# Kernel tuning notes

Hardware: AMD Instinct MI355X
Metric: run time of the kernel (lower is better)

Reference implementation:

```python
import jax, jax.numpy as jnp
import numpy as np

SEQ, BATCH = 256, 8
N_NODES = SEQ * BATCH
VOCAB, D_MODEL, H, D_K, D_FF, N_LAYERS, MAX_POS = 259, 256, 8, 32, 1024, 2, 128


def setup_inputs() -> dict:
    key = jax.random.key(0)
    ks = jax.random.split(key, 16)
    # structured causal edge list per sequence (dst attends to src <= dst, incl. self)
    tri_dst, tri_src = np.tril_indices(SEQ)
    offs = (np.arange(BATCH) * SEQ)[:, None]
    edge_src = jnp.asarray((tri_src[None, :] + offs).ravel(), dtype=jnp.int64)
    edge_dst = jnp.asarray((tri_dst[None, :] + offs).ravel(), dtype=jnp.int64)
    positions = jnp.tile(jnp.arange(SEQ, dtype=jnp.int64), BATCH)
    tokens = jax.random.randint(ks[0], (N_NODES,), 0, VOCAB, dtype=jnp.int64)
    s = 0.02
    p = lambda k, shp: jax.random.normal(k, shp, dtype=jnp.float32) * s
    return {
        "tokens": tokens, "positions": positions,
        "edge_src": edge_src, "edge_dst": edge_dst,
        "coord_emb": p(ks[1], (3, D_MODEL)),
        "pos_emb": p(ks[2], (MAX_POS, D_MODEL)),
        "value_emb": p(ks[3], (VOCAB, D_MODEL)),
        "ln1_scale": jnp.ones((N_LAYERS, D_MODEL)), "ln1_bias": jnp.zeros((N_LAYERS, D_MODEL)),
        "Wqkv": p(ks[4], (N_LAYERS, D_MODEL, 3 * D_MODEL)),
        "Wo": p(ks[5], (N_LAYERS, D_MODEL, D_MODEL)),
        "ln2_scale": jnp.ones((N_LAYERS, D_MODEL)), "ln2_bias": jnp.zeros((N_LAYERS, D_MODEL)),
        "W1": p(ks[6], (N_LAYERS, D_MODEL, D_FF)), "b1": jnp.zeros((N_LAYERS, D_FF)),
        "W2": p(ks[7], (N_LAYERS, D_FF, D_MODEL)), "b2": jnp.zeros((N_LAYERS, D_MODEL)),
        "lnf_scale": jnp.ones((D_MODEL,)), "lnf_bias": jnp.zeros((D_MODEL,)),
        "Wg": p(ks[8], (D_MODEL, VOCAB)), "bg": jnp.zeros((VOCAB,)),
    }


def _ln(x, scale, bias, eps=1e-5):
    mu = jnp.mean(x, axis=-1, keepdims=True)
    var = jnp.var(x, axis=-1, keepdims=True)
    return (x - mu) * jax.lax.rsqrt(var + eps) * scale + bias


def _graph_attention(x, src, dst, Wqkv, Wo, ln_s, ln_b):
    n = x.shape[0]
    xn = _ln(x, ln_s, ln_b)
    qkv = (xn @ Wqkv).reshape(n, 3, H, D_K)
    q, k, v = qkv[:, 0], qkv[:, 1], qkv[:, 2]  # [n, H, D_K] each
    # u_dot_v('k','q','score') per edge, scaled
    score = jnp.einsum("ehd,ehd->eh", k[src], q[dst]) / jnp.sqrt(jnp.float32(D_K))
    # edge_softmax over incoming edges of each dst node
    smax = jax.ops.segment_max(score, dst, num_segments=n)      # [n, H]
    ex = jnp.exp(score - smax[dst])                              # [E, H]
    denom = jax.ops.segment_sum(ex, dst, num_segments=n)        # [n, H]
    alpha = ex / denom[dst]
    # u_mul_e('v','softmax_score') + sum reduce -> z on dst nodes
    z = jax.ops.segment_sum(alpha[:, :, None] * v[src], dst, num_segments=n)  # [n, H, D_K]
    return x + z.reshape(n, D_MODEL) @ Wo


def reference(tokens, positions, edge_src, edge_dst, coord_emb, pos_emb, value_emb,
              ln1_scale, ln1_bias, Wqkv, Wo, ln2_scale, ln2_bias, W1, b1, W2, b2,
              lnf_scale, lnf_bias, Wg, bg):
    x = coord_emb[positions % 3] + pos_emb[positions // 3] + value_emb[tokens]
    for i in range(Wqkv.shape[0]):
        x = _graph_attention(x, edge_src, edge_dst, Wqkv[i], Wo[i], ln1_scale[i], ln1_bias[i])
        h = _ln(x, ln2_scale[i], ln2_bias[i])
        x = x + jax.nn.relu(h @ W1[i] + b1[i]) @ W2[i] + b2[i]
    out = _ln(x, lnf_scale, lnf_bias) @ Wg + bg
    return jax.nn.log_softmax(out, axis=-1)
```

## Files before the change

### kernel.cpp

```cpp
#include <hip/hip_runtime.h>
#include <hip/hip_bf16.h>

typedef __hip_bfloat16 bf16;
typedef unsigned short ushort_t;
typedef unsigned int uint_t;
typedef __attribute__((ext_vector_type(8))) short short8;
typedef __attribute__((ext_vector_type(4))) float floatx4;

#define D_MODEL 256
#define SEQ     256
#define BATCH   8
#define NN      2048
#define NHEAD   8
#define DK      32
#define DFF     1024
#define VOCAB   259
#define NLAYER  2

#define WQKVT_OFF 0
#define WOT_OFF   393216
#define W1T_OFF   524288
#define W2T_OFF   1048576
#define WGT_OFF   1572864
#define WT_TOTAL  1639168
// ... 143 lines not shown

template<bool BF, bool I64>
__device__ void prep_body(const void* tok, const void* pos,
        const void* ce, const void* pe, const void* ve,
        const void* Wqkv,
        const void* ln1s, const void* ln1b, const void* ln2s, const void* ln2b,
        const void* lnfs, const void* lnfb,
        const void* b1, const void* b2, const void* bg,
        ushort_t* WT, float* lnP, float* bP, float* x, ushort_t* xn,
        ushort_t (*tile)[72]) {
    int blk = blockIdx.x;
    if (blk < 48) {
        int lo = blk;
        ttile<BF>(Wqkv, 0, 256, 768, lo/12, lo%12, WT + WQKVT_OFF, tile);
    } else if (blk < 70) {
        int gid = (blk - 48) * 256 + threadIdx.x;
        if (gid < LNP_TOTAL) {
            float v;
            if      (gid < 512)  v = ldw<BF>(ln1s, gid);
            else if (gid < 1024) v = ldw<BF>(ln1b, gid - 512);
            else if (gid < 1536) v = ldw<BF>(ln2s, gid - 1024);
            else if (gid < 2048) v = ldw<BF>(ln2b, gid - 1536);
            else if (gid < 2304) v = ldw<BF>(lnfs, gid - 2048);
            else                 v = ldw<BF>(lnfb, gid - 2304);
            lnP[gid] = v;
        } else if (gid < LNP_TOTAL + BP_TOTAL) {
            int g = gid - LNP_TOTAL;
            float v;
            if      (g < 2048) v = ldw<BF>(b1, g);
            else if (g < 2560) v = ldw<BF>(b2, g - 2048);
            else               v = ldw<BF>(bg, g - 2560);
            bP[g] = v;
        }
    } else {
        embedln16<BF, I64>(tok, pos, ce, pe, ve, ln1s, ln1b, (blk - 70) * 16, x, xn);
    }
}

__global__ void __launch_bounds__(256) prep_k(const void* tok, const void* pos,
        const void* ce, const void* pe, const void* ve,
        const void* Wqkv,
        const void* ln1s, const void* ln1b, const void* ln2s, const void* ln2b,
        const void* lnfs, const void* lnfb,
        const void* b1, const void* b2, const void* bg,
        ushort_t* WT, float* lnP, float* bP, float* x, ushort_t* xn) {
    __shared__ ushort_t tile[64][72];
    bool BF = detBF(ln1s), I64 = detI64(pos);
    if (BF) { if (I64) prep_body<true,true >(tok,pos,ce,pe,ve,Wqkv,ln1s,ln1b,ln2s,ln2b,lnfs,lnfb,b1,b2,bg,WT,lnP,bP,x,xn,tile);
              else     prep_body<true,false>(tok,pos,ce,pe,ve,Wqkv,ln1s,ln1b,ln2s,ln2b,lnfs,lnfb,b1,b2,bg,WT,lnP,bP,x,xn,tile); }
    else    { if (I64) prep_body<false,true >(tok,pos,ce,pe,ve,Wqkv,ln1s,ln1b,ln2s,ln2b,lnfs,lnfb,b1,b2,bg,WT,lnP,bP,x,xn,tile);
              else     prep_body<false,false>(tok,pos,ce,pe,ve,Wqkv,ln1s,ln1b,ln2s,ln2b,lnfs,lnfb,b1,b2,bg,WT,lnP,bP,x,xn,tile); }
}

template<bool BF>
__device__ void qkvt_body(const ushort_t* __restrict__ xn,
        const ushort_t* __restrict__ WqkvT0, ushort_t* __restrict__ qkvB,
        const void* Wqkv, const void* Wo, const void* W1, const void* W2, const void* Wg,
        ushort_t* WT, ushort_t (*tile)[72]) {
    int bid = blockIdx.x;
    if (bid < 384) {
        int t = threadIdx.x;
        int lane = t & 63, wave = t >> 6;
        int quad = lane >> 4, l16 = lane & 15;
        int wm = (wave >> 1) * 32, wn = (wave & 1) * 32;
        int rowBase = (bid & 31) * 64, colBase = (bid >> 5) * 64;
        floatx4 acc[2][2];
        #pragma unroll
        for (int a = 0; a < 2; ++a)
            #pragma unroll
            for (int b = 0; b < 2; ++b) acc[a][b] = (floatx4){0.f,0.f,0.f,0.f};
        const ushort_t* a0 = xn + (size_t)(rowBase + wm + l16) * 256 + quad * 8;
        const ushort_t* a1 = a0 + (size_t)16 * 256;
        const ushort_t* b0 = WqkvT0 + (size_t)(colBase + wn + l16) * 256 + quad * 8;
        const ushort_t* b1 = b0 + (size_t)16 * 256;
        #pragma unroll 8
        for (int k0 = 0; k0 < 256; k0 += 32) {
            short8 af0 = *reinterpret_cast<const short8*>(a0 + k0);
            short8 af1 = *reinterpret_cast<const short8*>(a1 + k0);
            short8 bf0 = *reinterpret_cast<const short8*>(b0 + k0);
            short8 bf1 = *reinterpret_cast<const short8*>(b1 + k0);
            acc[0][0] = __builtin_amdgcn_mfma_f32_16x16x32_bf16(af0, bf0, acc[0][0], 0,0,0);
            acc[0][1] = __builtin_amdgcn_mfma_f32_16x16x32_bf16(af0, bf1, acc[0][1], 0,0,0);
            acc[1][0] = __builtin_amdgcn_mfma_f32_16x16x32_bf16(af1, bf0, acc[1][0], 0,0,0);
            acc[1][1] = __builtin_amdgcn_mfma_f32_16x16x32_bf16(af1, bf1, acc[1][1], 0,0,0);
        }
        #pragma unroll
        for (int nt = 0; nt < 2; ++nt) {
            int col = colBase + wn + nt*16 + l16;
            #pragma unroll
            for (int mt = 0; mt < 2; ++mt)
                #pragma unroll
                for (int r = 0; r < 4; ++r) {
                    int row = rowBase + wm + mt*16 + quad*4 + r;
                    qkvB[(size_t)row * 768 + col] = f2bs(acc[mt][nt][r]);
                }
        }
    } else {
        int task = bid - 384;
        const void* src; int K, N, tk, tn; size_t dstOff, srcOff;
        if (task < 48)       { int lo = task; src=Wqkv; K=256; N=768;
                               srcOff=196608; dstOff=WQKVT_OFF+196608;
                               tk=lo/12; tn=lo%12; }
        else if (task < 80)  { int t2=task-48, L=t2/16, lo=t2%16; src=Wo; K=256; N=256;
                               srcOff=(size_t)L*65536; dstOff=WOT_OFF+(size_t)L*65536;
                               tk=lo/4; tn=lo%4; }
        else if (task < 208) { int t2=task-80, L=t2/64, lo=t2%64; src=W1; K=256; N=1024;
                               srcOff=(size_t)L*262144; dstOff=W1T_OFF+(size_t)L*262144;
                               tk=lo/16; tn=lo%16; }
        else if (task < 336) { int t2=task-208, L=t2/64, lo=t2%64; src=W2; K=1024; N=256;
                               srcOff=(size_t)L*262144; dstOff=W2T_OFF+(size_t)L*262144;
                               tk=lo/4; tn=lo%4; }
        else                 { int lo=task-336; src=Wg; K=256; N=259;
                               srcOff=0; dstOff=WGT_OFF; tk=lo/5; tn=lo%5; }
        ttile<BF>(src, srcOff, K, N, tk, tn, WT + dstOff, tile);
    }
}

__global__ void __launch_bounds__(256) qkvt_k(const ushort_t* __restrict__ xn,
        const ushort_t* __restrict__ WqkvT0, ushort_t* __restrict__ qkvB,
        const void* Wqkv, const void* Wo, const void* W1, const void* W2, const void* Wg,
        ushort_t* WT, const void* ln1s) {
    __shared__ ushort_t tile[64][72];
    if (detBF(ln1s)) qkvt_body<true >(xn, WqkvT0, qkvB, Wqkv, Wo, W1, W2, Wg, WT, tile);
    else             qkvt_body<false>(xn, WqkvT0, qkvB, Wqkv, Wo, W1, W2, Wg, WT, tile);
}

union AttnSH {
    struct {
        ushort_t Ks[SEQ][40];
        ushort_t Qs[64][40];
    } a;
    ushort_t Ps[64][264];
};
__global__ void __launch_bounds__(256) attn_k(const ushort_t* __restrict__ qkvB,
                                              ushort_t* __restrict__ zB,
                                              float* __restrict__ yZ) {
    __shared__ AttnSH u;
    __shared__ ushort_t Vt[32][264];
    int t = threadIdx.x;
    {
        float4 z4 = make_float4(0.f, 0.f, 0.f, 0.f);
        float4* yp = reinterpret_cast<float4*>(yZ + (size_t)blockIdx.x * 2048);
        yp[t]       = z4;
        yp[t + 256] = z4;
    }
    int lane = t & 63, wave = t >> 6;
    int quad = lane >> 4, l16 = lane & 15;
    int tile = blockIdx.x & 3, bh = blockIdx.x >> 2;
    int b = bh >> 3, h = bh & 7;
    int base = b * SEQ;
    int dstBase = tile * 64;
    int tileEnd = (tile + 1) * 64;

    int nV = tileEnd * 4;
    for (int i = t; i < nV; i += 256) {
        int src = i >> 2, g = i & 3;
        const ushort_t* rp = qkvB + (size_t)(base + src) * 768 + h * 32 + g * 8;
        uint4 kv = *reinterpret_cast<const uint4*>(rp + 256);
        *reinterpret_cast<uint4*>(&u.a.Ks[src][g * 8]) = kv;
        uint4 vv = *reinterpret_cast<const uint4*>(rp + 512);
        const ushort_t* vs = (const ushort_t*)&vv;
        #pragma unroll
        for (int j = 0; j < 8; ++j) Vt[g * 8 + j][src] = vs[j];
    }
    {
        int r = t >> 2, g = t & 3;
        uint4 qv = *reinterpret_cast<const uint4*>(
            qkvB + (size_t)(base + dstBase + r) * 768 + h * 32 + g * 8);
        *reinterpret_cast<uint4*>(&u.a.Qs[r][g * 8]) = qv;
    }
    __syncthreads();

    const float scale = 0.17677669529663687f;
    int stLim = tile * 4 + wave;
    int stCnt = stLim + 1;
    short8 qf = *reinterpret_cast<const short8*>(&u.a.Qs[wave * 16 + l16][quad * 8]);
    floatx4 accs[16];
    #pragma unroll
    for (int st = 0; st < 16; ++st) {
        if (st <= stLim) {
            short8 kf = *reinterpret_cast<const short8*>(&u.a.Ks[st * 16 + l16][quad * 8]);
            accs[st] = __builtin_amdgcn_mfma_f32_16x16x32_bf16(qf, kf, (floatx4){0.f,0.f,0.f,0.f}, 0, 0, 0);
        }
    }
    float mrow[4] = {-3e38f, -3e38f, -3e38f, -3e38f};
    #pragma unroll
    for (int st = 0; st < 16; ++st) {
        if (st <= stLim) {
            int srcg = st * 16 + l16;
            #pragma unroll
            for (int r = 0; r < 4; ++r) {
                int dstg = dstBase + wave * 16 + quad * 4 + r;
                float sv = (srcg <= dstg) ? accs[st][r] * scale : -3e38f;
                accs[st][r] = sv;
                mrow[r] = fmaxf(mrow[r], sv);
            }
        }
    }
    #pragma unroll
    for (int mk = 1; mk < 16; mk <<= 1)
        #pragma unroll
        for (int r = 0; r < 4; ++r) mrow[r] = fmaxf(mrow[r], __shfl_xor(mrow[r], mk, 64));
    float lrow[4] = {0.f, 0.f, 0.f, 0.f};
    #pragma unroll
    for (int st = 0; st < 16; ++st) {
        if (st <= stLim) {
            #pragma unroll
            for (int r = 0; r < 4; ++r) {
                float p = __expf(accs[st][r] - mrow[r]);
                accs[st][r] = p;
                lrow[r] += p;
            }
        }
    }
    #pragma unroll
    for (int mk = 1; mk < 16; mk <<= 1)
        #pragma unroll
        for (int r = 0; r < 4; ++r) lrow[r] += __shfl_xor(lrow[r], mk, 64);
    __syncthreads();

    #pragma unroll
    for (int st = 0; st < 16; ++st) {
        if (st <= stLim) {
            #pragma unroll
            for (int r = 0; r < 4; ++r)
                u.Ps[wave * 16 + quad * 4 + r][st * 16 + l16] = f2bs(accs[st][r]);
        }
    }
    if (stCnt & 1) {
        #pragma unroll
        for (int r = 0; r < 4; ++r)
            u.Ps[wave * 16 + quad * 4 + r][stCnt * 16 + l16] = 0;
    }
    __syncthreads();

    int ktCnt = (stCnt + 1) >> 1;
    floatx4 acco[2];
    acco[0] = (floatx4){0.f,0.f,0.f,0.f};
    acco[1] = (floatx4){0.f,0.f,0.f,0.f};
    #pragma unroll
    for (int kt = 0; kt < 8; ++kt) {
        if (kt < ktCnt) {
            short8 pf = *reinterpret_cast<const short8*>(&u.Ps[wave * 16 + l16][kt * 32 + quad * 8]);
            #pragma unroll
            for (int dn = 0; dn < 2; ++dn) {
                short8 vf = *reinterpret_cast<const short8*>(&Vt[dn * 16 + l16][kt * 32 + quad * 8]);
                acco[dn] = __builtin_amdgcn_mfma_f32_16x16x32_bf16(pf, vf, acco[dn], 0, 0, 0);
            }
        }
    }
    #pragma unroll
    for (int dn = 0; dn < 2; ++dn)
        #pragma unroll
        for (int r = 0; r < 4; ++r)
            zB[(size_t)(base + dstBase + wave * 16 + quad * 4 + r) * 256
               + h * 32 + dn * 16 + l16] = f2bs(acco[dn][r] / lrow[r]);
}

__global__ void __launch_bounds__(256) tail_k(
        const ushort_t* __restrict__ zB, const ushort_t* __restrict__ WoT,
        const float* __restrict__ xIn,
        const float* __restrict__ ls2, const float* __restrict__ lb2,
        const ushort_t* __restrict__ W1T, const float* __restrict__ b1P,
        const ushort_t* __restrict__ W2T, const float* __restrict__ b2P,
        float* __restrict__ yAcc) {
    __shared__ float    xrowS[32][256];
    __shared__ ushort_t xnA[32][264];
    ushort_t (*hmidS)[264] = reinterpret_cast<ushort_t (*)[264]>(&xrowS[0][0]);
    int t = threadIdx.x, lane = t & 63, wave = t >> 6;
    int quad = lane >> 4, l16 = lane & 15;
    int rowBase = blockIdx.x * 32, cg = blockIdx.y;
    float vpre[2][4][4];

    {
        floatx4 acc[2][4];
        #pragma unroll
        for (int mt = 0; mt < 2; ++mt)
            #pragma unroll
            for (int nt = 0; nt < 4; ++nt) acc[mt][nt] = (floatx4){0.f,0.f,0.f,0.f};
        const ushort_t* a0 = zB + (size_t)(rowBase + l16) * 256 + quad * 8;
        const ushort_t* a1 = a0 + (size_t)16 * 256;
        #pragma unroll
        for (int k0 = 0; k0 < 256; k0 += 32) {
            short8 af0 = *reinterpret_cast<const short8*>(a0 + k0);
            short8 af1 = *reinterpret_cast<const short8*>(a1 + k0);
            #pragma unroll
            for (int nt = 0; nt < 4; ++nt) {
                short8 bv = *reinterpret_cast<const short8*>(
                    WoT + (size_t)(wave*64 + nt*16 + l16) * 256 + k0 + quad * 8);
                acc[0][nt] = __builtin_amdgcn_mfma_f32_16x16x32_bf16(af0, bv, acc[0][nt], 0,0,0);
                acc[1][nt] = __builtin_amdgcn_mfma_f32_16x16x32_bf16(af1, bv, acc[1][nt], 0,0,0);
            }
        }
        #pragma unroll
        for (int nt = 0; nt < 4; ++nt) {
            int col = wave*64 + nt*16 + l16;
            #pragma unroll
            for (int mt = 0; mt < 2; ++mt)
                #pragma unroll
                for (int r = 0; r < 4; ++r) {
                    int row = mt*16 + quad*4 + r;
                    float v = acc[mt][nt][r] + xIn[(size_t)(rowBase + row) * 256 + col];
                    vpre[mt][nt][r] = v;
                    xrowS[row][col] = v;
                }
        }
    }
    __syncthreads();
    #pragma unroll
    for (int i = 0; i < 8; ++i) {
        int row = wave*8 + i, c0 = lane * 4;
        float4 vv = *reinterpret_cast<const float4*>(&xrowS[row][c0]);
        float s  = wred_sum(vv.x + vv.y + vv.z + vv.w);
        float s2 = wred_sum(vv.x*vv.x + vv.y*vv.y + vv.z*vv.z + vv.w*vv.w);
        float mu = s * (1.f/256.f);
        float var = s2 * (1.f/256.f) - mu*mu;
        float rstd = rsqrtf(var + 1e-5f);
        ushort4 o;
        o.x = f2bs((vv.x-mu)*rstd*ls2[c0+0] + lb2[c0+0]);
        o.y = f2bs((vv.y-mu)*rstd*ls2[c0+1] + lb2[c0+1]);
        o.z = f2bs((vv.z-mu)*rstd*ls2[c0+2] + lb2[c0+2]);
        o.w = f2bs((vv.w-mu)*rstd*ls2[c0+3] + lb2[c0+3]);
        *reinterpret_cast<ushort4*>(&xnA[row][c0]) = o;
    }
    __syncthreads();
// ... 18 lines not shown
                acc[1][nt] = __builtin_amdgcn_mfma_f32_16x16x32_bf16(af1, bv, acc[1][nt], 0,0,0);
            }
        }
        __syncthreads();
        #pragma unroll
        for (int nt = 0; nt < 4; ++nt) {
            int lcol = wave*64 + nt*16 + l16;
            float bb = b1P[cg*256 + lcol];
            #pragma unroll
            for (int mt = 0; mt < 2; ++mt)
                #pragma unroll
                for (int r = 0; r < 4; ++r) {
                    int row = mt*16 + quad*4 + r;
                    hmidS[row][lcol] = f2bs(fmaxf(acc[mt][nt][r] + bb, 0.f));
                }
        }
    }
    __syncthreads();

    {
        floatx4 acc[2][4];
        #pragma unroll
        for (int mt = 0; mt < 2; ++mt)
            #pragma unroll
            for (int nt = 0; nt < 4; ++nt) acc[mt][nt] = (floatx4){0.f,0.f,0.f,0.f};
        const ushort_t* a0 = &hmidS[l16][quad * 8];
        const ushort_t* a1 = &hmidS[16 + l16][quad * 8];
        #pragma unroll
        for (int k0 = 0; k0 < 256; k0 += 32) {
            short8 af0 = *reinterpret_cast<const short8*>(a0 + k0);
            short8 af1 = *reinterpret_cast<const short8*>(a1 + k0);
            #pragma unroll
            for (int nt = 0; nt < 4; ++nt) {
                short8 bv = *reinterpret_cast<const short8*>(
                    W2T + (size_t)(wave*64 + nt*16 + l16) * 1024 + cg*256 + k0 + quad * 8);
                acc[0][nt] = __builtin_amdgcn_mfma_f32_16x16x32_bf16(af0, bv, acc[0][nt], 0,0,0);
                acc[1][nt] = __builtin_amdgcn_mfma_f32_16x16x32_bf16(af1, bv, acc[1][nt], 0,0,0);
            }
        }
        #pragma unroll
        for (int nt = 0; nt < 4; ++nt) {
            int col = wave*64 + nt*16 + l16;
            float bb = (cg == 0) ? b2P[col] : 0.f;
            #pragma unroll
            for (int mt = 0; mt < 2; ++mt)
                #pragma unroll
                for (int r = 0; r < 4; ++r) {
                    int row = mt*16 + quad*4 + r;
                    float add = acc[mt][nt][r];
                    if (cg == 0) add += vpre[mt][nt][r] + bb;
                    atomicAdd(&yAcc[(size_t)(rowBase + row) * 256 + col], add);
                }
        }
    }
}

__global__ void __launch_bounds__(256) lnqkv_k(
        const float* __restrict__ yIn,
        const float* __restrict__ ls, const float* __restrict__ lb,
        const ushort_t* __restrict__ WqkvT, ushort_t* __restrict__ qkvB) {
    __shared__ ushort_t xnA[64][264];
    int t = threadIdx.x, lane = t & 63, wave = t >> 6;
    int quad = lane >> 4, l16 = lane & 15;
    int rowBase = blockIdx.x * 64, colBase = blockIdx.y * 64;
    #pragma unroll
    for (int i = 0; i < 16; ++i) {
        int row = wave*16 + i, c0 = lane * 4;
        float4 vv = *reinterpret_cast<const float4*>(yIn + (size_t)(rowBase + row) * 256 + c0);
        float s  = wred_sum(vv.x + vv.y + vv.z + vv.w);
        float s2 = wred_sum(vv.x*vv.x + vv.y*vv.y + vv.z*vv.z + vv.w*vv.w);
        float mu = s * (1.f/256.f);
        float var = s2 * (1.f/256.f) - mu*mu;
        float rstd = rsqrtf(var + 1e-5f);
        ushort4 o;
        o.x = f2bs((vv.x-mu)*rstd*ls[c0+0] + lb[c0+0]);
        o.y = f2bs((vv.y-mu)*rstd*ls[c0+1] + lb[c0+1]);
        o.z = f2bs((vv.z-mu)*rstd*ls[c0+2] + lb[c0+2]);
        o.w = f2bs((vv.w-mu)*rstd*ls[c0+3] + lb[c0+3]);
        *reinterpret_cast<ushort4*>(&xnA[row][c0]) = o;
    }
    __syncthreads();
    int wm = (wave >> 1) * 32, wn = (wave & 1) * 32;
    floatx4 acc[2][2];
    #pragma unroll
    for (int a = 0; a < 2; ++a)
        #pragma unroll
        for (int b = 0; b < 2; ++b) acc[a][b] = (floatx4){0.f,0.f,0.f,0.f};
    const ushort_t* a0 = &xnA[wm + l16][quad * 8];
    const ushort_t* a1 = &xnA[wm + 16 + l16][quad * 8];
    #pragma unroll
    for (int k0 = 0; k0 < 256; k0 += 32) {
        short8 af0 = *reinterpret_cast<const short8*>(a0 + k0);
        short8 af1 = *reinterpret_cast<const short8*>(a1 + k0);
        #pragma unroll
        for (int nt = 0; nt < 2; ++nt) {
            short8 bv = *reinterpret_cast<const short8*>(
                WqkvT + (size_t)(colBase + wn + nt*16 + l16) * 256 + k0 + quad * 8);
            acc[0][nt] = __builtin_amdgcn_mfma_f32_16x16x32_bf16(af0, bv, acc[0][nt], 0,0,0);
            acc[1][nt] = __builtin_amdgcn_mfma_f32_16x16x32_bf16(af1, bv, acc[1][nt], 0,0,0);
        }
    }
    #pragma unroll
    for (int nt = 0; nt < 2; ++nt) {
        int col = colBase + wn + nt*16 + l16;
        #pragma unroll
        for (int mt = 0; mt < 2; ++mt)
            #pragma unroll
            for (int r = 0; r < 4; ++r) {
                int row = wm + mt*16 + quad*4 + r;
                qkvB[(size_t)(rowBase + row) * 768 + col] = f2bs(acc[mt][nt][r]);
            }
    }
}

__global__ void __launch_bounds__(256) lnlg_k(
        const float* __restrict__ yIn,
        const float* __restrict__ lnfsP, const float* __restrict__ lnfbP,
        const ushort_t* __restrict__ WgT, const float* __restrict__ bgP,
        const void* __restrict__ ln1sRaw, void* __restrict__ outp) {
    __shared__ float    xrow[16][256];
    __shared__ ushort_t xnA[16][264];
    __shared__ float    Lg[16][273];
    int t = threadIdx.x, lane = t & 63, wave = t >> 6;
    int quad = lane >> 4, l16 = lane & 15;
    int rowBase = blockIdx.x * 16;
    #pragma unroll
    for (int i = 0; i < 4; ++i) {
        int idx = i * 256 + t;
        int row = idx >> 6, c4 = (idx & 63) * 4;
        *reinterpret_cast<float4*>(&xrow[row][c4]) =
            *reinterpret_cast<const float4*>(yIn + (size_t)(rowBase + row) * 256 + c4);
    }
    __syncthreads();
    #pragma unroll
    for (int i = 0; i < 4; ++i) {
        int row = wave*4 + i, c0 = lane * 4;
        float4 vv = *reinterpret_cast<const float4*>(&xrow[row][c0]);
        float s  = wred_sum(vv.x + vv.y + vv.z + vv.w);
        float s2 = wred_sum(vv.x*vv.x + vv.y*vv.y + vv.z*vv.z + vv.w*vv.w);
        float mu = s * (1.f/256.f);
        float var = s2 * (1.f/256.f) - mu*mu;
        float rstd = rsqrtf(var + 1e-5f);
        ushort4 o;
        o.x = f2bs((vv.x-mu)*rstd*lnfsP[c0+0] + lnfbP[c0+0]);
        o.y = f2bs((vv.y-mu)*rstd*lnfsP[c0+1] + lnfbP[c0+1]);
        o.z = f2bs((vv.z-mu)*rstd*lnfsP[c0+2] + lnfbP[c0+2]);
        o.w = f2bs((vv.w-mu)*rstd*lnfsP[c0+3] + lnfbP[c0+3]);
        *reinterpret_cast<ushort4*>(&xnA[row][c0]) = o;
    }
    __syncthreads();
    const ushort_t* a0 = &xnA[l16][quad * 8];
    int cb = wave * 64;
    {
        floatx4 acc[4];
        #pragma unroll
        for (int nt = 0; nt < 4; ++nt) acc[nt] = (floatx4){0.f,0.f,0.f,0.f};
        #pragma unroll
        for (int kc = 0; kc < 8; ++kc) {
            short8 af = *reinterpret_cast<const short8*>(a0 + kc * 32);
            #pragma unroll
            for (int nt = 0; nt < 4; ++nt) {
                short8 bv = *reinterpret_cast<const short8*>(
                    WgT + (size_t)(cb + nt*16 + l16) * 256 + kc*32 + quad*8);
                acc[nt] = __builtin_amdgcn_mfma_f32_16x16x32_bf16(af, bv, acc[nt], 0,0,0);
// ... 31 lines not shown
        float v0 = Lg[row][lane],     v1 = Lg[row][lane+64];
        float v2 = Lg[row][lane+128], v3 = Lg[row][lane+192];
        float v4 = (lane < 16) ? Lg[row][256+lane] : -1e30f;
        float m = wred_max(fmaxf(fmaxf(fmaxf(v0,v1), fmaxf(v2,v3)), v4));
        float se = __expf(v0-m) + __expf(v1-m) + __expf(v2-m) + __expf(v3-m)
                 + ((lane < 16) ? __expf(v4-m) : 0.f);
        se = wred_sum(se);
        float lse = m + logf(se);
        size_t nbase = (size_t)(rowBase + row) * VOCAB;
        if (outBF) {
            ushort_t* o = (ushort_t*)outp + nbase;
            o[lane]     = f2bs(v0 - lse);
            o[lane+64]  = f2bs(v1 - lse);
            o[lane+128] = f2bs(v2 - lse);
            o[lane+192] = f2bs(v3 - lse);
            if (lane < 3) o[256+lane] = f2bs(v4 - lse);
        } else {
            float* o = (float*)outp + nbase;
            o[lane]     = v0 - lse;
            o[lane+64]  = v1 - lse;
            o[lane+128] = v2 - lse;
            o[lane+192] = v3 - lse;
            if (lane < 3) o[256+lane] = v4 - lse;
        }
    }
}

extern "C" void kernel_launch(void* const* d_in, const int* in_sizes, int n_in,
                              void* d_out, int out_size, void* d_ws, size_t ws_size,
                              hipStream_t stream) {
    const void* tok  = d_in[0];
    const void* pos  = d_in[1];
    const void* ce   = d_in[4];
    const void* pe   = d_in[5];
    const void* ve   = d_in[6];
    const void* ln1s = d_in[7];
    const void* ln1b = d_in[8];
    const void* Wqkv = d_in[9];
    const void* Wo   = d_in[10];
    const void* ln2s = d_in[11];
    const void* ln2b = d_in[12];
    const void* W1   = d_in[13];
    const void* b1   = d_in[14];
    const void* W2   = d_in[15];
    const void* b2   = d_in[16];
    const void* lnfs = d_in[17];
    const void* lnfb = d_in[18];
    const void* Wg   = d_in[19];
    const void* bg   = d_in[20];

    char* base = (char*)d_ws;
    float*    lnP   = (float*)base;
    float*    bP    = (float*)(base + 10240);
    float*    xA    = (float*)(base + 22528);
    ushort_t* xn    = (ushort_t*)(base + 2119680);
    ushort_t* zB    = (ushort_t*)(base + 3168256);
    ushort_t* WT    = (ushort_t*)(base + 8411136);
    ushort_t* qkvB  = (ushort_t*)(base + 11689472);
    float*    xB    = (float*)(base + 14835200);
    float*    xC    = (float*)(base + 16932352);

    prep_k<<<198, 256, 0, stream>>>(tok, pos, ce, pe, ve, Wqkv,
        ln1s, ln1b, ln2s, ln2b, lnfs, lnfb, b1, b2, bg, WT, lnP, bP, xA, xn);

    qkvt_k<<<740, 256, 0, stream>>>(xn, WT + WQKVT_OFF, qkvB,
        Wqkv, Wo, W1, W2, Wg, WT, ln1s);

    attn_k<<<256, 256, 0, stream>>>(qkvB, zB, xB);

    tail_k<<<dim3(64, 4), 256, 0, stream>>>(zB, WT + WOT_OFF, xA,
        lnP + 1024, lnP + 1536, WT + W1T_OFF, bP, WT + W2T_OFF, bP + 2048, xB);

    lnqkv_k<<<dim3(32, 12), 256, 0, stream>>>(xB, lnP + 256, lnP + 768,
        WT + WQKVT_OFF + 196608, qkvB);

    attn_k<<<256, 256, 0, stream>>>(qkvB, zB, xC);

    tail_k<<<dim3(64, 4), 256, 0, stream>>>(zB, WT + WOT_OFF + 65536, xB,
        lnP + 1024 + 256, lnP + 1536 + 256, WT + W1T_OFF + 262144, bP + 1024,
        WT + W2T_OFF + 262144, bP + 2048 + 256, xC);

    lnlg_k<<<128, 256, 0, stream>>>(xC, lnP + 2048, lnP + 2304,
        WT + WGT_OFF, bP + 2560, ln1s, d_out);
}
```

Measured before the change: 202.8 us.

## Fuse attention and tail kernels with per-tile atomic flags instead of launches

Attention and the Wo/FFN tail are merged into one persistent-style kernel of 512 blocks. The first 256 blocks run attention and signal per-(batch,tile) completion counters; the tail blocks spin on those counters before consuming z. The output accumulator zeroing moves into the preceding kernels (qkvt_k and lnqkv_k), which also reset the flags. This removes two kernel launch boundaries and lets tail work overlap attention, at the risk of deadlock if tail blocks occupy all slots before attention blocks are scheduled, plus spin overhead.

```diff
diff --git a/kernel.cpp b/kernel.cpp
--- a/kernel.cpp
+++ b/kernel.cpp
@@ -223,7 +223,8 @@
 __device__ void qkvt_body(const ushort_t* __restrict__ xn,
         const ushort_t* __restrict__ WqkvT0, ushort_t* __restrict__ qkvB,
         const void* Wqkv, const void* Wo, const void* W1, const void* W2, const void* Wg,
-        ushort_t* WT, ushort_t (*tile)[72]) {
+        ushort_t* WT, float* __restrict__ xBz, int* __restrict__ flags,
+        ushort_t (*tile)[72]) {
     int bid = blockIdx.x;
     if (bid < 384) {
         int t = threadIdx.x;
@@ -264,6 +265,13 @@
         }
     } else {
         int task = bid - 384;
+        if (task < 256) {
+            float4 z4 = make_float4(0.f, 0.f, 0.f, 0.f);
+            float4* yp = reinterpret_cast<float4*>(xBz + (size_t)task * 2048);
+            yp[threadIdx.x]       = z4;
+            yp[threadIdx.x + 256] = z4;
+        }
+        if (bid == 739 && threadIdx.x < 64) flags[threadIdx.x] = 0;
         const void* src; int K, N, tk, tn; size_t dstOff, srcOff;
         if (task < 48)       { int lo = task; src=Wqkv; K=256; N=768;
                                srcOff=196608; dstOff=WQKVT_OFF+196608;
@@ -286,10 +294,10 @@
 __global__ void __launch_bounds__(256) qkvt_k(const ushort_t* __restrict__ xn,
         const ushort_t* __restrict__ WqkvT0, ushort_t* __restrict__ qkvB,
         const void* Wqkv, const void* Wo, const void* W1, const void* W2, const void* Wg,
-        ushort_t* WT, const void* ln1s) {
+        ushort_t* WT, float* xBz, int* flags, const void* ln1s) {
     __shared__ ushort_t tile[64][72];
-    if (detBF(ln1s)) qkvt_body<true >(xn, WqkvT0, qkvB, Wqkv, Wo, W1, W2, Wg, WT, tile);
-    else             qkvt_body<false>(xn, WqkvT0, qkvB, Wqkv, Wo, W1, W2, Wg, WT, tile);
+    if (detBF(ln1s)) qkvt_body<true >(xn, WqkvT0, qkvB, Wqkv, Wo, W1, W2, Wg, WT, xBz, flags, tile);
+    else             qkvt_body<false>(xn, WqkvT0, qkvB, Wqkv, Wo, W1, W2, Wg, WT, xBz, flags, tile);
 }
 
 union AttnSH {
@@ -299,21 +307,20 @@
     } a;
     ushort_t Ps[64][264];
 };
-__global__ void __launch_bounds__(256) attn_k(const ushort_t* __restrict__ qkvB,
-                                              ushort_t* __restrict__ zB,
-                                              float* __restrict__ yZ) {
-    __shared__ AttnSH u;
-    __shared__ ushort_t Vt[32][264];
+union LayerSH {
+    struct { AttnSH u; ushort_t Vt[32][264]; } at;
+    struct { float xrowS[32][256]; ushort_t xnA[32][264]; } tl;
+};
+
+__device__ void attn_body(const ushort_t* __restrict__ qkvB,
+                          ushort_t* __restrict__ zB, int bid,
+                          int* __restrict__ flag, LayerSH& sh) {
+    AttnSH& u = sh.at.u;
+    ushort_t (*Vt)[264] = sh.at.Vt;
     int t = threadIdx.x;
-    {
-        float4 z4 = make_float4(0.f, 0.f, 0.f, 0.f);
-        float4* yp = reinterpret_cast<float4*>(yZ + (size_t)blockIdx.x * 2048);
-        yp[t]       = z4;
-        yp[t + 256] = z4;
-    }
     int lane = t & 63, wave = t >> 6;
     int quad = lane >> 4, l16 = lane & 15;
-    int tile = blockIdx.x & 3, bh = blockIdx.x >> 2;
+    int tile = bid & 3, bh = bid >> 2;
     int b = bh >> 3, h = bh & 7;
     int base = b * SEQ;
     int dstBase = tile * 64;
@@ -422,22 +429,39 @@
         for (int r = 0; r < 4; ++r)
             zB[(size_t)(base + dstBase + wave * 16 + quad * 4 + r) * 256
                + h * 32 + dn * 16 + l16] = f2bs(acco[dn][r] / lrow[r]);
-}
-
-__global__ void __launch_bounds__(256) tail_k(
-        const ushort_t* __restrict__ zB, const ushort_t* __restrict__ WoT,
-        const float* __restrict__ xIn,
+
+    __threadfence();
+    __syncthreads();
+    if (t == 0)
+        __hip_atomic_fetch_add(&flag[(b << 2) | tile], 1,
+                               __ATOMIC_RELEASE, __HIP_MEMORY_SCOPE_AGENT);
+}
+
+__device__ void tail_body(const ushort_t* __restrict__ zB,
+        const ushort_t* __restrict__ WoT, const float* __restrict__ xIn,
         const float* __restrict__ ls2, const float* __restrict__ lb2,
         const ushort_t* __restrict__ W1T, const float* __restrict__ b1P,
         const ushort_t* __restrict__ W2T, const float* __restrict__ b2P,
-        float* __restrict__ yAcc) {
-    __shared__ float    xrowS[32][256];
-    __shared__ ushort_t xnA[32][264];
+        float* __restrict__ yAcc, int bid2, int* __restrict__ flag, LayerSH& sh) {
+    float (*xrowS)[256] = sh.tl.xrowS;
+    ushort_t (*xnA)[264] = sh.tl.xnA;
     ushort_t (*hmidS)[264] = reinterpret_cast<ushort_t (*)[264]>(&xrowS[0][0]);
     int t = threadIdx.x, lane = t & 63, wave = t >> 6;
     int quad = lane >> 4, l16 = lane & 15;
-    int rowBase = blockIdx.x * 32, cg = blockIdx.y;
+    int rg = bid2 & 63, cg = bid2 >> 6;
+    int rowBase = rg * 32;
     float vpre[2][4][4];
+
+    {
+        int fidx = ((rg >> 3) << 2) | ((rg & 7) >> 1);
+        if (t == 0) {
+            while (__hip_atomic_load(&flag[fidx], __ATOMIC_RELAXED,
+                                     __HIP_MEMORY_SCOPE_AGENT) < 8)
+                __builtin_amdgcn_s_sleep(8);
+        }
+        __syncthreads();
+        __threadfence();
+    }
 
     {
         floatx4 acc[2][4];
@@ -565,13 +589,38 @@
     }
 }
 
+__global__ void __launch_bounds__(256) layer_k(
+        const ushort_t* __restrict__ qkvB, ushort_t* __restrict__ zB,
+        int* __restrict__ flag,
+        const ushort_t* __restrict__ WoT, const float* __restrict__ xIn,
+        const float* __restrict__ ls2, const float* __restrict__ lb2,
+        const ushort_t* __restrict__ W1T, const float* __restrict__ b1P,
+        const ushort_t* __restrict__ W2T, const float* __restrict__ b2P,
+        float* __restrict__ yAcc) {
+    __shared__ LayerSH sh;
+    int bid = blockIdx.x;
+    if (bid < 256)
+        attn_body(qkvB, zB, bid, flag, sh);
+    else
+        tail_body(zB, WoT, xIn, ls2, lb2, W1T, b1P, W2T, b2P, yAcc,
+                  bid - 256, flag, sh);
+}
+
 __global__ void __launch_bounds__(256) lnqkv_k(
         const float* __restrict__ yIn,
         const float* __restrict__ ls, const float* __restrict__ lb,
-        const ushort_t* __restrict__ WqkvT, ushort_t* __restrict__ qkvB) {
+        const ushort_t* __restrict__ WqkvT, ushort_t* __restrict__ qkvB,
+        float* __restrict__ xCz) {
     __shared__ ushort_t xnA[64][264];
     int t = threadIdx.x, lane = t & 63, wave = t >> 6;
     int quad = lane >> 4, l16 = lane & 15;
+    int lid = blockIdx.y * 32 + blockIdx.x;
+    if (lid < 256) {
+        float4 z4 = make_float4(0.f, 0.f, 0.f, 0.f);
+        float4* yp = reinterpret_cast<float4*>(xCz + (size_t)lid * 2048);
+        yp[t]       = z4;
+        yp[t + 256] = z4;
+    }
     int rowBase = blockIdx.x * 64, colBase = blockIdx.y * 64;
     #pragma unroll
     for (int i = 0; i < 16; ++i) {
@@ -757,6 +806,7 @@
     char* base = (char*)d_ws;
     float*    lnP   = (float*)base;
     float*    bP    = (float*)(base + 10240);
+    int*      flags = (int*)(base + 21760);
     float*    xA    = (float*)(base + 22528);
     ushort_t* xn    = (ushort_t*)(base + 2119680);
     ushort_t* zB    = (ushort_t*)(base + 3168256);
@@ -769,21 +819,18 @@
         ln1s, ln1b, ln2s, ln2b, lnfs, lnfb, b1, b2, bg, WT, lnP, bP, xA, xn);
 
     qkvt_k<<<740, 256, 0, stream>>>(xn, WT + WQKVT_OFF, qkvB,
-        Wqkv, Wo, W1, W2, Wg, WT, ln1s);
-
-    attn_k<<<256, 256, 0, stream>>>(qkvB, zB, xB);
-
-    tail_k<<<dim3(64, 4), 256, 0, stream>>>(zB, WT + WOT_OFF, xA,
-        lnP + 1024, lnP + 1536, WT + W1T_OFF, bP, WT + W2T_OFF, bP + 2048, xB);
+        Wqkv, Wo, W1, W2, Wg, WT, xB, flags, ln1s);
+
+    layer_k<<<512, 256, 0, stream>>>(qkvB, zB, flags,
+        WT + WOT_OFF, xA, lnP + 1024, lnP + 1536,
+        WT + W1T_OFF, bP, WT + W2T_OFF, bP + 2048, xB);
 
     lnqkv_k<<<dim3(32, 12), 256, 0, stream>>>(xB, lnP + 256, lnP + 768,
-        WT + WQKVT_OFF + 196608, qkvB);
-
-    attn_k<<<256, 256, 0, stream>>>(qkvB, zB, xC);
-
-    tail_k<<<dim3(64, 4), 256, 0, stream>>>(zB, WT + WOT_OFF + 65536, xB,
-        lnP + 1024 + 256, lnP + 1536 + 256, WT + W1T_OFF + 262144, bP + 1024,
-        WT + W2T_OFF + 262144, bP + 2048 + 256, xC);
+        WT + WQKVT_OFF + 196608, qkvB, xC);
+
+    layer_k<<<512, 256, 0, stream>>>(qkvB, zB, flags + 32,
+        WT + WOT_OFF + 65536, xB, lnP + 1280, lnP + 1792,
+        WT + W1T_OFF + 262144, bP + 1024, WT + W2T_OFF + 262144, bP + 2048 + 256, xC);
 
     lnlg_k<<<128, 256, 0, stream>>>(xC, lnP + 2048, lnP + 2304,
         WT + WGT_OFF, bP + 2560, ln1s, d_out);
```

After: 294.5 us. 1.45x slower.

## Fuse QKV projection (and layer-2 LayerNorm) into the attention kernel

Applied to the files above, without the earlier changes.

Each attention block now computes its own K, V (and Q for its tile) for the head it owns, directly into shared memory, using MFMA over the normalized input. The separate QKV GEMM kernels and the qkvB round trip through global memory go away, which removes two launches. Layer 2 also fuses the LayerNorm into the attention block. The cost is redundant work: causal tiles of the same batch and head recompute overlapping K/V rows, so total FLOPs rise and the load on later tiles becomes uneven.

```diff
diff --git a/kernel.cpp b/kernel.cpp
--- a/kernel.cpp
+++ b/kernel.cpp
@@ -219,134 +219,110 @@
               else     prep_body<false,false>(tok,pos,ce,pe,ve,Wqkv,ln1s,ln1b,ln2s,ln2b,lnfs,lnfb,b1,b2,bg,WT,lnP,bP,x,xn,tile); }
 }
 
-template<bool BF>
-__device__ void qkvt_body(const ushort_t* __restrict__ xn,
-        const ushort_t* __restrict__ WqkvT0, ushort_t* __restrict__ qkvB,
-        const void* Wqkv, const void* Wo, const void* W1, const void* W2, const void* Wg,
-        ushort_t* WT, ushort_t (*tile)[72]) {
-    int bid = blockIdx.x;
-    if (bid < 384) {
-        int t = threadIdx.x;
-        int lane = t & 63, wave = t >> 6;
-        int quad = lane >> 4, l16 = lane & 15;
-        int wm = (wave >> 1) * 32, wn = (wave & 1) * 32;
-        int rowBase = (bid & 31) * 64, colBase = (bid >> 5) * 64;
-        floatx4 acc[2][2];
-        #pragma unroll
-        for (int a = 0; a < 2; ++a)
-            #pragma unroll
-            for (int b = 0; b < 2; ++b) acc[a][b] = (floatx4){0.f,0.f,0.f,0.f};
-        const ushort_t* a0 = xn + (size_t)(rowBase + wm + l16) * 256 + quad * 8;
-        const ushort_t* a1 = a0 + (size_t)16 * 256;
-        const ushort_t* b0 = WqkvT0 + (size_t)(colBase + wn + l16) * 256 + quad * 8;
-        const ushort_t* b1 = b0 + (size_t)16 * 256;
-        #pragma unroll 8
-        for (int k0 = 0; k0 < 256; k0 += 32) {
-            short8 af0 = *reinterpret_cast<const short8*>(a0 + k0);
-            short8 af1 = *reinterpret_cast<const short8*>(a1 + k0);
-            short8 bf0 = *reinterpret_cast<const short8*>(b0 + k0);
-            short8 bf1 = *reinterpret_cast<const short8*>(b1 + k0);
-            acc[0][0] = __builtin_amdgcn_mfma_f32_16x16x32_bf16(af0, bf0, acc[0][0], 0,0,0);
-            acc[0][1] = __builtin_amdgcn_mfma_f32_16x16x32_bf16(af0, bf1, acc[0][1], 0,0,0);
-            acc[1][0] = __builtin_amdgcn_mfma_f32_16x16x32_bf16(af1, bf0, acc[1][0], 0,0,0);
-            acc[1][1] = __builtin_amdgcn_mfma_f32_16x16x32_bf16(af1, bf1, acc[1][1], 0,0,0);
-        }
-        #pragma unroll
-        for (int nt = 0; nt < 2; ++nt) {
-            int col = colBase + wn + nt*16 + l16;
-            #pragma unroll
-            for (int mt = 0; mt < 2; ++mt)
-                #pragma unroll
-                for (int r = 0; r < 4; ++r) {
-                    int row = rowBase + wm + mt*16 + quad*4 + r;
-                    qkvB[(size_t)row * 768 + col] = f2bs(acc[mt][nt][r]);
-                }
-        }
-    } else {
-        int task = bid - 384;
-        const void* src; int K, N, tk, tn; size_t dstOff, srcOff;
-        if (task < 48)       { int lo = task; src=Wqkv; K=256; N=768;
-                               srcOff=196608; dstOff=WQKVT_OFF+196608;
-                               tk=lo/12; tn=lo%12; }
-        else if (task < 80)  { int t2=task-48, L=t2/16, lo=t2%16; src=Wo; K=256; N=256;
-                               srcOff=(size_t)L*65536; dstOff=WOT_OFF+(size_t)L*65536;
-                               tk=lo/4; tn=lo%4; }
-        else if (task < 208) { int t2=task-80, L=t2/64, lo=t2%64; src=W1; K=256; N=1024;
-                               srcOff=(size_t)L*262144; dstOff=W1T_OFF+(size_t)L*262144;
-                               tk=lo/16; tn=lo%16; }
-        else if (task < 336) { int t2=task-208, L=t2/64, lo=t2%64; src=W2; K=1024; N=256;
-                               srcOff=(size_t)L*262144; dstOff=W2T_OFF+(size_t)L*262144;
-                               tk=lo/4; tn=lo%4; }
-        else                 { int lo=task-336; src=Wg; K=256; N=259;
-                               srcOff=0; dstOff=WGT_OFF; tk=lo/5; tn=lo%5; }
-        ttile<BF>(src, srcOff, K, N, tk, tn, WT + dstOff, tile);
-    }
-}
-
-__global__ void __launch_bounds__(256) qkvt_k(const ushort_t* __restrict__ xn,
-        const ushort_t* __restrict__ WqkvT0, ushort_t* __restrict__ qkvB,
-        const void* Wqkv, const void* Wo, const void* W1, const void* W2, const void* Wg,
-        ushort_t* WT, const void* ln1s) {
-    __shared__ ushort_t tile[64][72];
-    if (detBF(ln1s)) qkvt_body<true >(xn, WqkvT0, qkvB, Wqkv, Wo, W1, W2, Wg, WT, tile);
-    else             qkvt_body<false>(xn, WqkvT0, qkvB, Wqkv, Wo, W1, W2, Wg, WT, tile);
-}
-
-union AttnSH {
-    struct {
-        ushort_t Ks[SEQ][40];
-        ushort_t Qs[64][40];
-    } a;
-    ushort_t Ps[64][264];
-};
-__global__ void __launch_bounds__(256) attn_k(const ushort_t* __restrict__ qkvB,
-                                              ushort_t* __restrict__ zB,
-                                              float* __restrict__ yZ) {
-    __shared__ AttnSH u;
-    __shared__ ushort_t Vt[32][264];
+#define SMEM_USHORTS 29696
+
+template<int LN>
+__device__ void attnq_body(const ushort_t* __restrict__ xnG,
+        const float* __restrict__ yIn,
+        const float* __restrict__ ls, const float* __restrict__ lb,
+        const ushort_t* __restrict__ WqkvT,
+        ushort_t* __restrict__ zB, int bid, ushort_t* smem) {
+    ushort_t (*Ks)[40]   = reinterpret_cast<ushort_t (*)[40]>(smem);
+    ushort_t (*Qs)[40]   = reinterpret_cast<ushort_t (*)[40]>(smem + 10240);
+    ushort_t (*xnC)[264] = reinterpret_cast<ushort_t (*)[264]>(smem + 12800);
+    ushort_t (*Ps)[264]  = reinterpret_cast<ushort_t (*)[264]>(smem);
+    ushort_t (*Vt)[264]  = reinterpret_cast<ushort_t (*)[264]>(smem + 21248);
+
     int t = threadIdx.x;
-    {
-        float4 z4 = make_float4(0.f, 0.f, 0.f, 0.f);
-        float4* yp = reinterpret_cast<float4*>(yZ + (size_t)blockIdx.x * 2048);
-        yp[t]       = z4;
-        yp[t + 256] = z4;
-    }
     int lane = t & 63, wave = t >> 6;
     int quad = lane >> 4, l16 = lane & 15;
-    int tile = blockIdx.x & 3, bh = blockIdx.x >> 2;
+    int tile = bid & 3, bh = bid >> 2;
     int b = bh >> 3, h = bh & 7;
     int base = b * SEQ;
     int dstBase = tile * 64;
     int tileEnd = (tile + 1) * 64;
 
-    int nV = tileEnd * 4;
-    for (int i = t; i < nV; i += 256) {
-        int src = i >> 2, g = i & 3;
-        const ushort_t* rp = qkvB + (size_t)(base + src) * 768 + h * 32 + g * 8;
-        uint4 kv = *reinterpret_cast<const uint4*>(rp + 256);
-        *reinterpret_cast<uint4*>(&u.a.Ks[src][g * 8]) = kv;
-        uint4 vv = *reinterpret_cast<const uint4*>(rp + 512);
-        const ushort_t* vs = (const ushort_t*)&vv;
-        #pragma unroll
-        for (int j = 0; j < 8; ++j) Vt[g * 8 + j][src] = vs[j];
-    }
-    {
-        int r = t >> 2, g = t & 3;
-        uint4 qv = *reinterpret_cast<const uint4*>(
-            qkvB + (size_t)(base + dstBase + r) * 768 + h * 32 + g * 8);
-        *reinterpret_cast<uint4*>(&u.a.Qs[r][g * 8]) = qv;
+    int nsc = tileEnd >> 5;
+    int rcl = wave >> 1, isV = wave & 1;
+    int rowLocal = rcl * 16 + l16;
+    int kvColBase = (isV ? 512 : 256) + h * 32;
+    const ushort_t* bk0 = WqkvT + (size_t)(kvColBase + l16) * 256 + quad * 8;
+    const ushort_t* bk1 = WqkvT + (size_t)(kvColBase + 16 + l16) * 256 + quad * 8;
+    int qct = wave & 1;
+    const ushort_t* bq = WqkvT + (size_t)(h * 32 + qct * 16 + l16) * 256 + quad * 8;
+
+    for (int sc = 0; sc < nsc; ++sc) {
+        if (LN) {
+            #pragma unroll
+            for (int i = 0; i < 8; ++i) {
+                int lr = wave * 8 + i;
+                int c0 = lane * 4;
+                float4 vv = *reinterpret_cast<const float4*>(
+                    yIn + (size_t)(base + sc*32 + lr) * 256 + c0);
+                float s  = wred_sum(vv.x + vv.y + vv.z + vv.w);
+                float s2 = wred_sum(vv.x*vv.x + vv.y*vv.y + vv.z*vv.z + vv.w*vv.w);
+                float mu = s * (1.f/256.f);
+                float var = s2 * (1.f/256.f) - mu*mu;
+                float rstd = rsqrtf(var + 1e-5f);
+                ushort4 o;
+                o.x = f2bs((vv.x-mu)*rstd*ls[c0+0] + lb[c0+0]);
+                o.y = f2bs((vv.y-mu)*rstd*ls[c0+1] + lb[c0+1]);
+                o.z = f2bs((vv.z-mu)*rstd*ls[c0+2] + lb[c0+2]);
+                o.w = f2bs((vv.w-mu)*rstd*ls[c0+3] + lb[c0+3]);
+                *reinterpret_cast<ushort4*>(&xnC[lr][c0]) = o;
+            }
+            __syncthreads();
+        }
+        const ushort_t* aP = LN ? &xnC[rowLocal][quad * 8]
+                                : xnG + (size_t)(base + sc*32 + rowLocal) * 256 + quad * 8;
+        int qsc = sc - 2 * tile;
+        floatx4 acc0 = (floatx4){0.f,0.f,0.f,0.f};
+        floatx4 acc1 = (floatx4){0.f,0.f,0.f,0.f};
+        floatx4 accq = (floatx4){0.f,0.f,0.f,0.f};
+        #pragma unroll
+        for (int k0 = 0; k0 < 256; k0 += 32) {
+            short8 af = *reinterpret_cast<const short8*>(aP + k0);
+            short8 b0 = *reinterpret_cast<const short8*>(bk0 + k0);
+            short8 b1 = *reinterpret_cast<const short8*>(bk1 + k0);
+            acc0 = __builtin_amdgcn_mfma_f32_16x16x32_bf16(af, b0, acc0, 0,0,0);
+            acc1 = __builtin_amdgcn_mfma_f32_16x16x32_bf16(af, b1, acc1, 0,0,0);
+            if (qsc >= 0) {
+                short8 bb = *reinterpret_cast<const short8*>(bq + k0);
+                accq = __builtin_amdgcn_mfma_f32_16x16x32_bf16(af, bb, accq, 0,0,0);
+            }
+        }
+        int srow = sc*32 + rcl*16;
+        if (!isV) {
+            #pragma unroll
+            for (int r = 0; r < 4; ++r) {
+                Ks[srow + quad*4 + r][l16]      = f2bs(acc0[r]);
+                Ks[srow + quad*4 + r][16 + l16] = f2bs(acc1[r]);
+            }
+        } else {
+            #pragma unroll
+            for (int r = 0; r < 4; ++r) {
+                Vt[l16][srow + quad*4 + r]      = f2bs(acc0[r]);
+                Vt[16 + l16][srow + quad*4 + r] = f2bs(acc1[r]);
+            }
+        }
+        if (qsc >= 0) {
+            #pragma unroll
+            for (int r = 0; r < 4; ++r)
+                Qs[qsc*32 + rcl*16 + quad*4 + r][qct*16 + l16] = f2bs(accq[r]);
+        }
+        if (LN) __syncthreads();
     }
     __syncthreads();
 
     const float scale = 0.17677669529663687f;
     int stLim = tile * 4 + wave;
     int stCnt = stLim + 1;
-    short8 qf = *reinterpret_cast<const short8*>(&u.a.Qs[wave * 16 + l16][quad * 8]);
+    short8 qf = *reinterpret_cast<const short8*>(&Qs[wave * 16 + l16][quad * 8]);
     floatx4 accs[16];
     #pragma unroll
     for (int st = 0; st < 16; ++st) {
         if (st <= stLim) {
-            short8 kf = *reinterpret_cast<const short8*>(&u.a.Ks[st * 16 + l16][quad * 8]);
+            short8 kf = *reinterpret_cast<const short8*>(&Ks[st * 16 + l16][quad * 8]);
             accs[st] = __builtin_amdgcn_mfma_f32_16x16x32_bf16(qf, kf, (floatx4){0.f,0.f,0.f,0.f}, 0, 0, 0);
         }
     }
@@ -391,13 +367,13 @@
         if (st <= stLim) {
             #pragma unroll
             for (int r = 0; r < 4; ++r)
-                u.Ps[wave * 16 + quad * 4 + r][st * 16 + l16] = f2bs(accs[st][r]);
+                Ps[wave * 16 + quad * 4 + r][st * 16 + l16] = f2bs(accs[st][r]);
         }
     }
     if (stCnt & 1) {
         #pragma unroll
         for (int r = 0; r < 4; ++r)
-            u.Ps[wave * 16 + quad * 4 + r][stCnt * 16 + l16] = 0;
+            Ps[wave * 16 + quad * 4 + r][stCnt * 16 + l16] = 0;
     }
     __syncthreads();
 
@@ -408,7 +384,7 @@
     #pragma unroll
     for (int kt = 0; kt < 8; ++kt) {
         if (kt < ktCnt) {
-            short8 pf = *reinterpret_cast<const short8*>(&u.Ps[wave * 16 + l16][kt * 32 + quad * 8]);
+            short8 pf = *reinterpret_cast<const short8*>(&Ps[wave * 16 + l16][kt * 32 + quad * 8]);
             #pragma unroll
             for (int dn = 0; dn < 2; ++dn) {
                 short8 vf = *reinterpret_cast<const short8*>(&Vt[dn * 16 + l16][kt * 32 + quad * 8]);
@@ -422,6 +398,66 @@
         for (int r = 0; r < 4; ++r)
             zB[(size_t)(base + dstBase + wave * 16 + quad * 4 + r) * 256
                + h * 32 + dn * 16 + l16] = f2bs(acco[dn][r] / lrow[r]);
+}
+
+template<bool BF>
+__device__ void attnq0_aux(int task, const void* Wqkv, const void* Wo,
+        const void* W1, const void* W2, const void* Wg,
+        ushort_t* WT, float* xBz, ushort_t (*tile)[72]) {
+    if (task < 256) {
+        float4 z4 = make_float4(0.f, 0.f, 0.f, 0.f);
+        float4* yp = reinterpret_cast<float4*>(xBz + (size_t)task * 2048);
+        yp[threadIdx.x]       = z4;
+        yp[threadIdx.x + 256] = z4;
+    }
+    const void* src; int K, N, tk, tn; size_t dstOff, srcOff;
+    if (task < 48)       { int lo = task; src=Wqkv; K=256; N=768;
+                           srcOff=196608; dstOff=WQKVT_OFF+196608;
+                           tk=lo/12; tn=lo%12; }
+    else if (task < 80)  { int t2=task-48, L=t2/16, lo=t2%16; src=Wo; K=256; N=256;
+                           srcOff=(size_t)L*65536; dstOff=WOT_OFF+(size_t)L*65536;
+                           tk=lo/4; tn=lo%4; }
+    else if (task < 208) { int t2=task-80, L=t2/64, lo=t2%64; src=W1; K=256; N=1024;
+                           srcOff=(size_t)L*262144; dstOff=W1T_OFF+(size_t)L*262144;
+                           tk=lo/16; tn=lo%16; }
+    else if (task < 336) { int t2=task-208, L=t2/64, lo=t2%64; src=W2; K=1024; N=256;
+                           srcOff=(size_t)L*262144; dstOff=W2T_OFF+(size_t)L*262144;
+                           tk=lo/4; tn=lo%4; }
+    else                 { int lo=task-336; src=Wg; K=256; N=259;
+                           srcOff=0; dstOff=WGT_OFF; tk=lo/5; tn=lo%5; }
+    ttile<BF>(src, srcOff, K, N, tk, tn, WT + dstOff, tile);
+}
+
+__global__ void __launch_bounds__(256) attnq0_k(const ushort_t* __restrict__ xn,
+        const ushort_t* __restrict__ WqkvT0, ushort_t* __restrict__ zB,
+        const void* Wqkv, const void* Wo, const void* W1, const void* W2, const void* Wg,
+        ushort_t* WT, float* xBz, const void* ln1s) {
+    __shared__ ushort_t smem[SMEM_USHORTS];
+    int bid = blockIdx.x;
+    if (bid < 256) {
+        attnq_body<0>(xn, nullptr, nullptr, nullptr, WqkvT0, zB, bid, smem);
+    } else {
+        ushort_t (*tile)[72] = reinterpret_cast<ushort_t (*)[72]>(smem);
+        if (detBF(ln1s)) attnq0_aux<true >(bid - 256, Wqkv, Wo, W1, W2, Wg, WT, xBz, tile);
+        else             attnq0_aux<false>(bid - 256, Wqkv, Wo, W1, W2, Wg, WT, xBz, tile);
+    }
+}
+
+__global__ void __launch_bounds__(256) attnq1_k(const float* __restrict__ yIn,
+        const float* __restrict__ ls, const float* __restrict__ lb,
+        const ushort_t* __restrict__ WqkvT1, ushort_t* __restrict__ zB,
+        float* __restrict__ xCz) {
+    __shared__ ushort_t smem[SMEM_USHORTS];
+    int bid = blockIdx.x;
+    if (bid < 256) {
+        attnq_body<1>(nullptr, yIn, ls, lb, WqkvT1, zB, bid, smem);
+    } else {
+        int task = bid - 256;
+        float4 z4 = make_float4(0.f, 0.f, 0.f, 0.f);
+        float4* yp = reinterpret_cast<float4*>(xCz + (size_t)task * 2048);
+        yp[threadIdx.x]       = z4;
+        yp[threadIdx.x + 256] = z4;
+    }
 }
 
 __global__ void __launch_bounds__(256) tail_k(
@@ -562,64 +598,6 @@
                     atomicAdd(&yAcc[(size_t)(rowBase + row) * 256 + col], add);
                 }
         }
-    }
-}
-
-__global__ void __launch_bounds__(256) lnqkv_k(
-        const float* __restrict__ yIn,
-        const float* __restrict__ ls, const float* __restrict__ lb,
-        const ushort_t* __restrict__ WqkvT, ushort_t* __restrict__ qkvB) {
-    __shared__ ushort_t xnA[64][264];
-    int t = threadIdx.x, lane = t & 63, wave = t >> 6;
-    int quad = lane >> 4, l16 = lane & 15;
-    int rowBase = blockIdx.x * 64, colBase = blockIdx.y * 64;
-    #pragma unroll
-    for (int i = 0; i < 16; ++i) {
-        int row = wave*16 + i, c0 = lane * 4;
-        float4 vv = *reinterpret_cast<const float4*>(yIn + (size_t)(rowBase + row) * 256 + c0);
-        float s  = wred_sum(vv.x + vv.y + vv.z + vv.w);
-        float s2 = wred_sum(vv.x*vv.x + vv.y*vv.y + vv.z*vv.z + vv.w*vv.w);
-        float mu = s * (1.f/256.f);
-        float var = s2 * (1.f/256.f) - mu*mu;
-        float rstd = rsqrtf(var + 1e-5f);
-        ushort4 o;
-        o.x = f2bs((vv.x-mu)*rstd*ls[c0+0] + lb[c0+0]);
-        o.y = f2bs((vv.y-mu)*rstd*ls[c0+1] + lb[c0+1]);
-        o.z = f2bs((vv.z-mu)*rstd*ls[c0+2] + lb[c0+2]);
-        o.w = f2bs((vv.w-mu)*rstd*ls[c0+3] + lb[c0+3]);
-        *reinterpret_cast<ushort4*>(&xnA[row][c0]) = o;
-    }
-    __syncthreads();
-    int wm = (wave >> 1) * 32, wn = (wave & 1) * 32;
-    floatx4 acc[2][2];
-    #pragma unroll
-    for (int a = 0; a < 2; ++a)
-        #pragma unroll
-        for (int b = 0; b < 2; ++b) acc[a][b] = (floatx4){0.f,0.f,0.f,0.f};
-    const ushort_t* a0 = &xnA[wm + l16][quad * 8];
-    const ushort_t* a1 = &xnA[wm + 16 + l16][quad * 8];
-    #pragma unroll
-    for (int k0 = 0; k0 < 256; k0 += 32) {
-        short8 af0 = *reinterpret_cast<const short8*>(a0 + k0);
-        short8 af1 = *reinterpret_cast<const short8*>(a1 + k0);
-        #pragma unroll
-        for (int nt = 0; nt < 2; ++nt) {
-            short8 bv = *reinterpret_cast<const short8*>(
-                WqkvT + (size_t)(colBase + wn + nt*16 + l16) * 256 + k0 + quad * 8);
-            acc[0][nt] = __builtin_amdgcn_mfma_f32_16x16x32_bf16(af0, bv, acc[0][nt], 0,0,0);
-            acc[1][nt] = __builtin_amdgcn_mfma_f32_16x16x32_bf16(af1, bv, acc[1][nt], 0,0,0);
-        }
-    }
-    #pragma unroll
-    for (int nt = 0; nt < 2; ++nt) {
-        int col = colBase + wn + nt*16 + l16;
-        #pragma unroll
-        for (int mt = 0; mt < 2; ++mt)
-            #pragma unroll
-            for (int r = 0; r < 4; ++r) {
-                int row = wm + mt*16 + quad*4 + r;
-                qkvB[(size_t)(rowBase + row) * 768 + col] = f2bs(acc[mt][nt][r]);
-            }
     }
 }
 
@@ -761,28 +739,23 @@
     ushort_t* xn    = (ushort_t*)(base + 2119680);
     ushort_t* zB    = (ushort_t*)(base + 3168256);
     ushort_t* WT    = (ushort_t*)(base + 8411136);
-    ushort_t* qkvB  = (ushort_t*)(base + 11689472);
     float*    xB    = (float*)(base + 14835200);
     float*    xC    = (float*)(base + 16932352);
 
     prep_k<<<198, 256, 0, stream>>>(tok, pos, ce, pe, ve, Wqkv,
         ln1s, ln1b, ln2s, ln2b, lnfs, lnfb, b1, b2, bg, WT, lnP, bP, xA, xn);
 
-    qkvt_k<<<740, 256, 0, stream>>>(xn, WT + WQKVT_OFF, qkvB,
-        Wqkv, Wo, W1, W2, Wg, WT, ln1s);
-
-    attn_k<<<256, 256, 0, stream>>>(qkvB, zB, xB);
+    attnq0_k<<<612, 256, 0, stream>>>(xn, WT + WQKVT_OFF, zB,
+        Wqkv, Wo, W1, W2, Wg, WT, xB, ln1s);
 
     tail_k<<<dim3(64, 4), 256, 0, stream>>>(zB, WT + WOT_OFF, xA,
         lnP + 1024, lnP + 1536, WT + W1T_OFF, bP, WT + W2T_OFF, bP + 2048, xB);
 
-    lnqkv_k<<<dim3(32, 12), 256, 0, stream>>>(xB, lnP + 256, lnP + 768,
-        WT + WQKVT_OFF + 196608, qkvB);
-
-    attn_k<<<256, 256, 0, stream>>>(qkvB, zB, xC);
+    attnq1_k<<<512, 256, 0, stream>>>(xB, lnP + 256, lnP + 768,
+        WT + WQKVT_OFF + 196608, zB, xC);
 
     tail_k<<<dim3(64, 4), 256, 0, stream>>>(zB, WT + WOT_OFF + 65536, xB,
-        lnP + 1024 + 256, lnP + 1536 + 256, WT + W1T_OFF + 262144, bP + 1024,
+        lnP + 1280, lnP + 1792, WT + W1T_OFF + 262144, bP + 1024,
         WT + W2T_OFF + 262144, bP + 2048 + 256, xC);
 
     lnlg_k<<<128, 256, 0, stream>>>(xC, lnP + 2048, lnP + 2304,
```

Result: slower. 216.8 us (+6.9%).
